# Performance work log

Hardware: AMD Instinct MI355X
Metric: run time of the kernel (lower is better)

## Reference

```python
import jax, jax.numpy as jnp
import numpy as np

NUM_CLASSES = 32
TRI = NUM_CLASSES * (NUM_CLASSES - 1) // 2      # 496 class pairs
HID = 32 * TRI                                  # 15872 total hidden
IN = 512
B = 256
RATIO = 0.0

# pair -> (i, j) class indices, in the same enumeration order as the torch idx formula
_I_IDX, _J_IDX = np.triu_indices(NUM_CLASSES, k=1)
_I_IDX = jnp.asarray(_I_IDX)
_J_IDX = jnp.asarray(_J_IDX)


def setup_inputs() -> dict:
    key = jax.random.key(0)
    ks = jax.random.split(key, 7)
    s = 0.02  # small init so activations stay sane
    return {
        "x": jax.random.normal(ks[0], (B, IN), jnp.float32),
        "W1": jax.random.normal(ks[1], (IN, HID), jnp.float32) * s,
        "b1": jax.random.normal(ks[2], (HID,), jnp.float32) * s,
        "W2": jax.random.normal(ks[3], (HID, HID), jnp.float32) * s,
        "b2": jax.random.normal(ks[4], (HID,), jnp.float32) * s,
        "Wout": jax.random.normal(ks[5], (HID, 2 * TRI), jnp.float32) * s,
        "bout": jax.random.normal(ks[6], (2 * TRI,), jnp.float32) * s,
    }


def reference(x, W1, b1, W2, b2, Wout, bout):
    # MLP stack: fc1 + relu, fc2 + relu (num_layers=2), fc_out
    h = jax.nn.relu(x @ W1 + b1)                 # [B, HID]
    h = jax.nn.relu(h @ W2 + b2)                 # [B, HID]
    out = h @ Wout + bout                        # [B, 2*TRI]

    # vote scatter: out[:, 2p], out[:, 2p+1] are the (i, j) logits of pair p
    pair = out.reshape(B, TRI, 2)                # [B, TRI, 2]
    d = pair[..., 0] - pair[..., 1]              # [B, TRI]
    # original condition: d > ratio  OR  -d >= ratio   (always true at ratio=0)
    mask = (d > RATIO) | (-d >= RATIO)
    vi = jnp.where(mask, pair[..., 0], 0.0)      # contribution to class i
    vj = jnp.where(mask, pair[..., 1], 0.0)      # contribution to class j

    votes = jnp.zeros((B, NUM_CLASSES), jnp.float32)
    votes = votes.at[:, _I_IDX].add(vi)
    votes = votes.at[:, _J_IDX].add(vj)
    return votes
```

## Files before the change

kernel.cpp:

```cpp
#include <hip/hip_runtime.h>
#include <hip/hip_bf16.h>

using short8 = __attribute__((ext_vector_type(8))) short;
using f32x16 = __attribute__((ext_vector_type(16))) float;
using us4    = __attribute__((ext_vector_type(4))) unsigned short;

#define NHID 15872

__device__ __forceinline__ unsigned short f2bf(float f) {
  unsigned u = __builtin_bit_cast(unsigned, f);
  u += 0x7fff + ((u >> 16) & 1);
  return (unsigned short)(u >> 16);
}
__device__ __forceinline__ short f2bf_hw(float f) {
  __hip_bfloat16 h = __float2bfloat16(f);
  return __builtin_bit_cast(short, h);
}
__device__ __forceinline__ float bf2f(unsigned short h) {
  return __builtin_bit_cast(float, ((unsigned)h) << 16);
}

__device__ __forceinline__ void gload16(const void* g, void* l) {
  __builtin_amdgcn_global_load_lds(
      (const __attribute__((address_space(1))) unsigned int*)g,
      (__attribute__((address_space(3))) unsigned int*)l, 16, 0, 0);
}

__device__ __forceinline__ size_t pk_idx(int row, int col) {
  return (size_t)(col >> 4) * 4096 +
         (size_t)(row + 256 * ((col >> 3) & 1)) * 8 + (col & 7);
}

__global__ void cvt_x_pack(const float* __restrict__ x, unsigned short* __restrict__ xpk) {
  int g = blockIdx.x * 256 + threadIdx.x;
  int row = g >> 6, k0 = (g & 63) * 8;
  const float* p = x + (size_t)row * 512 + k0;
  float4 a = *reinterpret_cast<const float4*>(p);
  float4 b = *reinterpret_cast<const float4*>(p + 4);
  us4 o0, o1;
  o0[0] = f2bf(a.x); o0[1] = f2bf(a.y); o0[2] = f2bf(a.z); o0[3] = f2bf(a.w);
  o1[0] = f2bf(b.x); o1[1] = f2bf(b.y); o1[2] = f2bf(b.z); o1[3] = f2bf(b.w);
  unsigned short* d = xpk + pk_idx(row, k0);
  *reinterpret_cast<us4*>(d)     = o0;
  *reinterpret_cast<us4*>(d + 4) = o1;
}


#define WAITV(N) asm volatile("s_waitcnt vmcnt(" #N ")" ::: "memory")

#define STAGEB(BUF, T) do { \
    gload16(bsrc + (size_t)(T) * 32 * NHID,       &Blds[BUF][(w * 4 + 0) * 128]); \
    gload16(bsrc + ((size_t)(T) * 32 + 2) * NHID, &Blds[BUF][(w * 4 + 2) * 128]); \
  } while (0)

#define LOADA(T) do { \
    const unsigned short* ap_ = asrc + (size_t)(T) * 8192; \
    rA[0] = *reinterpret_cast<const short8*>(ap_); \
    rA[1] = *reinterpret_cast<const short8*>(ap_ + 4096); \
    rA[2] = *reinterpret_cast<const short8*>(ap_ + 256); \
    rA[3] = *reinterpret_cast<const short8*>(ap_ + 4096 + 256); \
  } while (0)

#define COMPUTE(BC) do { \
    const float* bb_ = &Blds[BC][0]; \
    _Pragma("unroll") \
    for (int ks_ = 0; ks_ < 2; ++ks_) { \
      short8 bfr_[2]; \
      _Pragma("unroll") \
      for (int nb_ = 0; nb_ < 2; ++nb_) { \
        float tf_[8]; \
        _Pragma("unroll") \
        for (int jj_ = 0; jj_ < 8; ++jj_) \
          tf_[jj_] = bb_[(ks_ * 16 + hi * 8 + jj_) * 128 + wn * 64 + nb_ * 32 + l31]; \
        _Pragma("unroll") \
        for (int jj_ = 0; jj_ < 8; ++jj_) bfr_[nb_][jj_] = f2bf_hw(tf_[jj_]); \
      } \
      acc[0] = __builtin_amdgcn_mfma_f32_32x32x16_bf16(rA[ks_],     bfr_[0], acc[0], 0, 0, 0); \
      acc[1] = __builtin_amdgcn_mfma_f32_32x32x16_bf16(rA[ks_],     bfr_[1], acc[1], 0, 0, 0); \
      acc[2] = __builtin_amdgcn_mfma_f32_32x32x16_bf16(rA[2 + ks_], bfr_[0], acc[2], 0, 0, 0); \
      acc[3] = __builtin_amdgcn_mfma_f32_32x32x16_bf16(rA[2 + ks_], bfr_[1], acc[3], 0, 0, 0); \
    } \
  } while (0)

template<int OUTMODE, bool SWZ>
__global__ __launch_bounds__(512, 4)
void gemm_v12(const unsigned short* __restrict__ Apk, int KC,
              const float* __restrict__ B, const float* __restrict__ bias,
              unsigned short* __restrict__ Cf, float* __restrict__ Cp)
{
  __shared__ float Blds[3][32 * 128];

  int nidx, ks0;
  if (SWZ) {
    int b = blockIdx.x;
    int xcd = b & 7;
    ks0  = xcd >> 1;
    nidx = (b >> 3) * 2 + (xcd & 1);
  } else {
    nidx = blockIdx.x; ks0 = blockIdx.y;
  }
  const int n0   = nidx * 128;
  const int k0   = ks0 * KC;
  const int tid  = threadIdx.x;
  const int w    = tid >> 6;
  const int lane = tid & 63;
  const int l31  = lane & 31;
  const int hi   = lane >> 5;
  const int wm   = w >> 1;
  const int wn   = w & 1;

  f32x16 acc[4] = {};
  short8 rA[4];

  const float* bsrc = B + (size_t)(k0 + w * 4 + hi) * NHID + n0 + l31 * 4;
  const unsigned short* asrc = Apk + (size_t)(k0 >> 4) * 4096 +
                               (size_t)(wm * 64 + l31 + 256 * hi) * 8;

  const int NT = KC >> 5;

  STAGEB(0, 0);
  STAGEB(1, 1);

  int bc = 0;
  for (int t = 0; t < NT; ++t) {
    if (t + 1 < NT) { WAITV(2); } else { WAITV(0); }
    __builtin_amdgcn_sched_barrier(0);
    __builtin_amdgcn_s_barrier();
    LOADA(t);
    if (t + 2 < NT) { int sb_ = bc >= 1 ? bc - 1 : 2; STAGEB(sb_, t + 2); }
    COMPUTE(bc);
    bc = bc == 2 ? 0 : bc + 1;
  }

#pragma unroll
  for (int rb = 0; rb < 2; ++rb) {
#pragma unroll
    for (int nb = 0; nb < 2; ++nb) {
      int col = n0 + wn * 64 + nb * 32 + l31;
      float bv = (OUTMODE != 1) ? bias[col] : 0.f;
#pragma unroll
      for (int reg = 0; reg < 16; ++reg) {
        int row = wm * 64 + rb * 32 + (reg & 3) + 8 * (reg >> 2) + 4 * hi;
        float v = acc[rb * 2 + nb][reg];
        if (OUTMODE == 0) {
          v += bv; v = v > 0.f ? v : 0.f;
          Cf[pk_idx(row, col)] = f2bf(v);
        } else if (OUTMODE == 1) {
          Cp[(size_t)ks0 * 256 * NHID + (size_t)row * NHID + col] = v;
        } else {
          v += bv; v = v > 0.f ? v : 0.f;
          Cf[(size_t)row * NHID + col] = f2bf(v);
        }
      }
    }
  }
}

template<bool PACK>
__global__ void reduce_h(const float* __restrict__ part, const float* __restrict__ bias,
                         unsigned short* __restrict__ out, int S) {
  int g4 = blockIdx.x * 256 + threadIdx.x;
  int row = g4 / 3968;
  int c   = (g4 - row * 3968) * 4;
  size_t off = (size_t)row * NHID + c;
  float4 s = *reinterpret_cast<const float4*>(part + off);
  for (int k = 1; k < S; ++k) {
    float4 p = *reinterpret_cast<const float4*>(part + (size_t)k * 256 * NHID + off);
    s.x += p.x; s.y += p.y; s.z += p.z; s.w += p.w;
  }
  float4 b = *reinterpret_cast<const float4*>(bias + c);
  s.x += b.x; s.y += b.y; s.z += b.z; s.w += b.w;
  us4 o;
  o[0] = f2bf(s.x > 0.f ? s.x : 0.f);
  o[1] = f2bf(s.y > 0.f ? s.y : 0.f);
  o[2] = f2bf(s.z > 0.f ? s.z : 0.f);
  o[3] = f2bf(s.w > 0.f ? s.w : 0.f);
  if (PACK) *reinterpret_cast<us4*>(out + pk_idx(row, c)) = o;
  else      *reinterpret_cast<us4*>(out + off) = o;
}

__global__ void wv_fold(const float* __restrict__ Wout, float* __restrict__ Wv) {
  int g = blockIdx.x * 256 + threadIdx.x;
  int k = g >> 5, c = g & 31;
  const float* row = Wout + (size_t)k * 992;
  float s = 0.f;
#pragma unroll
  for (int o = 0; o < 32; ++o) {
    if (o == c) continue;
    int i = c < o ? c : o;
    int j = c < o ? o : c;
    int p = 31 * i - (i * (i - 1)) / 2 + (j - i - 1);
    s += row[2 * p + (c > o ? 1 : 0)];
  }
  Wv[g] = s;
}

__global__ void votes_partial(const unsigned short* __restrict__ h2,
                              const float* __restrict__ Wv,
                              float* __restrict__ part) {
  int bm = blockIdx.x >> 5;
  int ks = blockIdx.x & 31;
  int r  = bm * 8 + (threadIdx.x >> 5);
  int c  = threadIdx.x & 31;
  const unsigned short* hrow = h2 + (size_t)r * NHID + ks * 496;
  const float* wp = Wv + (size_t)(ks * 496) * 32 + c;
  float s = 0.f;
  for (int k0 = 0; k0 < 496; k0 += 8) {
    short8 hv = *reinterpret_cast<const short8*>(hrow + k0);
#pragma unroll
    for (int j = 0; j < 8; ++j)
      s += bf2f((unsigned short)hv[j]) * wp[(size_t)(k0 + j) * 32];
  }
  part[(size_t)(ks * 256 + r) * 32 + c] = s;
}

__global__ void votes_reduce(const float* __restrict__ part,
                             const float* __restrict__ bout,
                             float* __restrict__ out) {
  int g = blockIdx.x * 256 + threadIdx.x;
  int c = g & 31;
  float s = 0.f;
#pragma unroll
  for (int ks = 0; ks < 32; ++ks) s += part[(size_t)ks * 8192 + g];
  float bv = 0.f;
#pragma unroll
  for (int o = 0; o < 32; ++o) {
    if (o == c) continue;
    int i = c < o ? c : o;
    int j = c < o ? o : c;
    int p = 31 * i - (i * (i - 1)) / 2 + (j - i - 1);
    bv += bout[2 * p + (c > o ? 1 : 0)];
  }
  out[g] = s + bv;
}

extern "C" void kernel_launch(void* const* d_in, const int* in_sizes, int n_in,
                              void* d_out, int out_size, void* d_ws, size_t ws_size,
                              hipStream_t stream) {
  const float* x    = (const float*)d_in[0];
  const float* W1   = (const float*)d_in[1];
  const float* b1   = (const float*)d_in[2];
  const float* W2   = (const float*)d_in[3];
  const float* b2   = (const float*)d_in[4];
  const float* Wout = (const float*)d_in[5];
  const float* bout = (const float*)d_in[6];
  float* out = (float*)d_out;

  char* ws = (char*)d_ws;
  unsigned short* xpk  = (unsigned short*)(ws);
  unsigned short* h1pk = (unsigned short*)(ws + 262144);
  unsigned short* h2   = (unsigned short*)(ws + 8388608);
  float*          Wv   = (float*)(ws + 16515072);
  float*          part = (float*)(ws + 18546688);
  float*         part2 = (float*)(ws + 19595264);

  const size_t PART1 = (size_t)256 * NHID * 4;
  const bool split = ws_size >= 19595264ull + 4 * PART1;

  hipLaunchKernelGGL(cvt_x_pack, dim3(64), dim3(256), 0, stream, x, xpk);
  if (split) {
    hipLaunchKernelGGL((gemm_v12<1, false>), dim3(124, 2), dim3(512), 0, stream,
                       xpk, 256, W1, (const float*)nullptr,
                       (unsigned short*)nullptr, part2);
    hipLaunchKernelGGL((reduce_h<true>), dim3(3968), dim3(256), 0, stream,
                       part2, b1, h1pk, 2);
    hipLaunchKernelGGL((gemm_v12<1, true>), dim3(496), dim3(512), 0, stream,
                       h1pk, 3968, W2, (const float*)nullptr,
                       (unsigned short*)nullptr, part2);
    hipLaunchKernelGGL((reduce_h<false>), dim3(3968), dim3(256), 0, stream,
                       part2, b2, h2, 4);
  } else {
    hipLaunchKernelGGL((gemm_v12<0, false>), dim3(124, 1), dim3(512), 0, stream,
                       xpk, 512, W1, b1, h1pk, (float*)nullptr);
    hipLaunchKernelGGL((gemm_v12<2, false>), dim3(124, 1), dim3(512), 0, stream,
                       h1pk, NHID, W2, b2, h2, (float*)nullptr);
  }
  hipLaunchKernelGGL(wv_fold,       dim3(1984), dim3(256), 0, stream, Wout, Wv);
  hipLaunchKernelGGL(votes_partial, dim3(1024), dim3(256), 0, stream, h2, Wv, part);
  hipLaunchKernelGGL(votes_reduce,  dim3(32),   dim3(256), 0, stream, part, bout, out);
}
```

Measured before the change: 394.0 us.

## Retile GEMM to 128x256 block tiles with K-step 16 and M split

Changes the GEMM block tile from 256 rows x 128 columns to 128 rows x 256 columns, splitting M across a new grid dimension and reducing the K step per stage from 32 to 16. LDS buffers are padded (BSTRIDE) and the B staging pattern now loads two full 256-wide K rows per wave. Each fp32 W row segment is loaded wider and more contiguously, so fewer blocks share a column strip. The trade-off is that each B tile is now read by two M-half blocks, and the pipeline runs more iterations with less MFMA work per barrier.

```diff
diff --git a/kernel.cpp b/kernel.cpp
--- a/kernel.cpp
+++ b/kernel.cpp
@@ -48,75 +48,74 @@
 
 #define WAITV(N) asm volatile("s_waitcnt vmcnt(" #N ")" ::: "memory")
 
+#define BSTRIDE 4736
+
 #define STAGEB(BUF, T) do { \
-    gload16(bsrc + (size_t)(T) * 32 * NHID,       &Blds[BUF][(w * 4 + 0) * 128]); \
-    gload16(bsrc + ((size_t)(T) * 32 + 2) * NHID, &Blds[BUF][(w * 4 + 2) * 128]); \
+    gload16(bsrc + (size_t)(T) * 16 * NHID,       &Blds[(BUF) * BSTRIDE + (2 * w) * 256]); \
+    gload16(bsrc + ((size_t)(T) * 16 + 1) * NHID, &Blds[(BUF) * BSTRIDE + (2 * w + 1) * 256]); \
   } while (0)
 
 #define LOADA(T) do { \
-    const unsigned short* ap_ = asrc + (size_t)(T) * 8192; \
+    const unsigned short* ap_ = asrc + (size_t)(T) * 4096; \
     rA[0] = *reinterpret_cast<const short8*>(ap_); \
-    rA[1] = *reinterpret_cast<const short8*>(ap_ + 4096); \
-    rA[2] = *reinterpret_cast<const short8*>(ap_ + 256); \
-    rA[3] = *reinterpret_cast<const short8*>(ap_ + 4096 + 256); \
+    rA[1] = *reinterpret_cast<const short8*>(ap_ + 256); \
   } while (0)
 
 #define COMPUTE(BC) do { \
-    const float* bb_ = &Blds[BC][0]; \
+    const float* bb_ = &Blds[(BC) * BSTRIDE]; \
+    short8 bfr_[2]; \
     _Pragma("unroll") \
-    for (int ks_ = 0; ks_ < 2; ++ks_) { \
-      short8 bfr_[2]; \
+    for (int nb_ = 0; nb_ < 2; ++nb_) { \
+      float tf_[8]; \
       _Pragma("unroll") \
-      for (int nb_ = 0; nb_ < 2; ++nb_) { \
-        float tf_[8]; \
-        _Pragma("unroll") \
-        for (int jj_ = 0; jj_ < 8; ++jj_) \
-          tf_[jj_] = bb_[(ks_ * 16 + hi * 8 + jj_) * 128 + wn * 64 + nb_ * 32 + l31]; \
-        _Pragma("unroll") \
-        for (int jj_ = 0; jj_ < 8; ++jj_) bfr_[nb_][jj_] = f2bf_hw(tf_[jj_]); \
-      } \
-      acc[0] = __builtin_amdgcn_mfma_f32_32x32x16_bf16(rA[ks_],     bfr_[0], acc[0], 0, 0, 0); \
-      acc[1] = __builtin_amdgcn_mfma_f32_32x32x16_bf16(rA[ks_],     bfr_[1], acc[1], 0, 0, 0); \
-      acc[2] = __builtin_amdgcn_mfma_f32_32x32x16_bf16(rA[2 + ks_], bfr_[0], acc[2], 0, 0, 0); \
-      acc[3] = __builtin_amdgcn_mfma_f32_32x32x16_bf16(rA[2 + ks_], bfr_[1], acc[3], 0, 0, 0); \
+      for (int jj_ = 0; jj_ < 8; ++jj_) \
+        tf_[jj_] = bb_[(hi * 8 + jj_) * 256 + wn * 64 + nb_ * 32 + l31]; \
+      _Pragma("unroll") \
+      for (int jj_ = 0; jj_ < 8; ++jj_) bfr_[nb_][jj_] = f2bf_hw(tf_[jj_]); \
     } \
+    acc[0] = __builtin_amdgcn_mfma_f32_32x32x16_bf16(rA[0], bfr_[0], acc[0], 0, 0, 0); \
+    acc[1] = __builtin_amdgcn_mfma_f32_32x32x16_bf16(rA[0], bfr_[1], acc[1], 0, 0, 0); \
+    acc[2] = __builtin_amdgcn_mfma_f32_32x32x16_bf16(rA[1], bfr_[0], acc[2], 0, 0, 0); \
+    acc[3] = __builtin_amdgcn_mfma_f32_32x32x16_bf16(rA[1], bfr_[1], acc[3], 0, 0, 0); \
   } while (0)
 
 template<int OUTMODE, bool SWZ>
 __global__ __launch_bounds__(512, 4)
-void gemm_v12(const unsigned short* __restrict__ Apk, int KC,
+void gemm_v13(const unsigned short* __restrict__ Apk, int KC,
               const float* __restrict__ B, const float* __restrict__ bias,
               unsigned short* __restrict__ Cf, float* __restrict__ Cp)
 {
-  __shared__ float Blds[3][32 * 128];
-
-  int nidx, ks0;
+  __shared__ float Blds[3 * BSTRIDE];
+
+  int nidx, ks0, mh;
   if (SWZ) {
-    int b = blockIdx.x;
-    int xcd = b & 7;
+    int xs = blockIdx.x;
+    int xcd = xs & 7;
     ks0  = xcd >> 1;
-    nidx = (b >> 3) * 2 + (xcd & 1);
+    nidx = (xs >> 3) * 2 + (xcd & 1);
+    mh   = blockIdx.y;
+    if (nidx >= 62) return;
   } else {
-    nidx = blockIdx.x; ks0 = blockIdx.y;
-  }
-  const int n0   = nidx * 128;
+    nidx = blockIdx.x; mh = blockIdx.y; ks0 = blockIdx.z;
+  }
+  const int n0   = nidx * 256;
   const int k0   = ks0 * KC;
   const int tid  = threadIdx.x;
   const int w    = tid >> 6;
   const int lane = tid & 63;
   const int l31  = lane & 31;
   const int hi   = lane >> 5;
-  const int wm   = w >> 1;
-  const int wn   = w & 1;
+  const int wm   = w >> 2;
+  const int wn   = w & 3;
 
   f32x16 acc[4] = {};
-  short8 rA[4];
-
-  const float* bsrc = B + (size_t)(k0 + w * 4 + hi) * NHID + n0 + l31 * 4;
+  short8 rA[2];
+
+  const float* bsrc = B + (size_t)(k0 + 2 * w) * NHID + n0 + lane * 4;
   const unsigned short* asrc = Apk + (size_t)(k0 >> 4) * 4096 +
-                               (size_t)(wm * 64 + l31 + 256 * hi) * 8;
-
-  const int NT = KC >> 5;
+                               (size_t)(mh * 128 + wm * 64 + l31 + 256 * hi) * 8;
+
+  const int NT = KC >> 4;
 
   STAGEB(0, 0);
   STAGEB(1, 1);
@@ -140,7 +139,7 @@
       float bv = (OUTMODE != 1) ? bias[col] : 0.f;
 #pragma unroll
       for (int reg = 0; reg < 16; ++reg) {
-        int row = wm * 64 + rb * 32 + (reg & 3) + 8 * (reg >> 2) + 4 * hi;
+        int row = mh * 128 + wm * 64 + rb * 32 + (reg & 3) + 8 * (reg >> 2) + 4 * hi;
         float v = acc[rb * 2 + nb][reg];
         if (OUTMODE == 0) {
           v += bv; v = v > 0.f ? v : 0.f;
@@ -259,20 +258,20 @@
 
   hipLaunchKernelGGL(cvt_x_pack, dim3(64), dim3(256), 0, stream, x, xpk);
   if (split) {
-    hipLaunchKernelGGL((gemm_v12<1, false>), dim3(124, 2), dim3(512), 0, stream,
+    hipLaunchKernelGGL((gemm_v13<1, false>), dim3(62, 2, 2), dim3(512), 0, stream,
                        xpk, 256, W1, (const float*)nullptr,
                        (unsigned short*)nullptr, part2);
     hipLaunchKernelGGL((reduce_h<true>), dim3(3968), dim3(256), 0, stream,
                        part2, b1, h1pk, 2);
-    hipLaunchKernelGGL((gemm_v12<1, true>), dim3(496), dim3(512), 0, stream,
+    hipLaunchKernelGGL((gemm_v13<1, true>), dim3(256, 2), dim3(512), 0, stream,
                        h1pk, 3968, W2, (const float*)nullptr,
                        (unsigned short*)nullptr, part2);
     hipLaunchKernelGGL((reduce_h<false>), dim3(3968), dim3(256), 0, stream,
                        part2, b2, h2, 4);
   } else {
-    hipLaunchKernelGGL((gemm_v12<0, false>), dim3(124, 1), dim3(512), 0, stream,
+    hipLaunchKernelGGL((gemm_v13<0, false>), dim3(62, 2, 1), dim3(512), 0, stream,
                        xpk, 512, W1, b1, h1pk, (float*)nullptr);
-    hipLaunchKernelGGL((gemm_v12<2, false>), dim3(124, 1), dim3(512), 0, stream,
+    hipLaunchKernelGGL((gemm_v13<2, false>), dim3(62, 2, 1), dim3(512), 0, stream,
                        h1pk, NHID, W2, b2, h2, (float*)nullptr);
   }
   hipLaunchKernelGGL(wv_fold,       dim3(1984), dim3(256), 0, stream, Wout, Wv);
```

Result: slower. 441.5 us (+12.1%).

## Use 4-wave blocks with 64x128 warp tiles, 16-way split-K, bf16 partials

Applied to the files above, without the earlier changes.

The GEMM moves from 8 waves per block to 4, so each wave computes 64 rows by all 128 columns with 8 accumulators and issues four B staging loads per tile. The W2 GEMM now splits K 16 ways over 1984 blocks instead of 4 ways over 496. Split-K partials are stored as bf16, which halves the partial traffic, and the reduction kernel sums eight elements per thread. The aim is more parallelism in the large GEMM and less partial-sum bandwidth, at the cost of more partial reads in the reduction, extra rounding error from bf16 partials, and higher register pressure. The wait count is now a fixed vmcnt(4) on every iteration, including the last tile.

```diff
diff --git a/kernel.cpp b/kernel.cpp
--- a/kernel.cpp
+++ b/kernel.cpp
@@ -48,10 +48,11 @@
 
 #define WAITV(N) asm volatile("s_waitcnt vmcnt(" #N ")" ::: "memory")
 
-#define STAGEB(BUF, T) do { \
-    gload16(bsrc + (size_t)(T) * 32 * NHID,       &Blds[BUF][(w * 4 + 0) * 128]); \
-    gload16(bsrc + ((size_t)(T) * 32 + 2) * NHID, &Blds[BUF][(w * 4 + 2) * 128]); \
-  } while (0)
+#define STAGEB(BUF, T) do { _Pragma("unroll") \
+  for (int j_ = 0; j_ < 4; ++j_) \
+    gload16(bsrc + ((size_t)(T) * 32 + 2 * j_) * NHID, \
+            &Blds[BUF][(w * 8 + 2 * j_) * 128]); \
+} while (0)
 
 #define LOADA(T) do { \
     const unsigned short* ap_ = asrc + (size_t)(T) * 8192; \
@@ -65,37 +66,34 @@
     const float* bb_ = &Blds[BC][0]; \
     _Pragma("unroll") \
     for (int ks_ = 0; ks_ < 2; ++ks_) { \
-      short8 bfr_[2]; \
       _Pragma("unroll") \
-      for (int nb_ = 0; nb_ < 2; ++nb_) { \
+      for (int nb_ = 0; nb_ < 4; ++nb_) { \
         float tf_[8]; \
         _Pragma("unroll") \
         for (int jj_ = 0; jj_ < 8; ++jj_) \
-          tf_[jj_] = bb_[(ks_ * 16 + hi * 8 + jj_) * 128 + wn * 64 + nb_ * 32 + l31]; \
+          tf_[jj_] = bb_[(ks_ * 16 + hi * 8 + jj_) * 128 + nb_ * 32 + l31]; \
+        short8 bfr_; \
         _Pragma("unroll") \
-        for (int jj_ = 0; jj_ < 8; ++jj_) bfr_[nb_][jj_] = f2bf_hw(tf_[jj_]); \
+        for (int jj_ = 0; jj_ < 8; ++jj_) bfr_[jj_] = f2bf_hw(tf_[jj_]); \
+        acc[nb_]     = __builtin_amdgcn_mfma_f32_32x32x16_bf16(rA[ks_],     bfr_, acc[nb_],     0, 0, 0); \
+        acc[4 + nb_] = __builtin_amdgcn_mfma_f32_32x32x16_bf16(rA[2 + ks_], bfr_, acc[4 + nb_], 0, 0, 0); \
       } \
-      acc[0] = __builtin_amdgcn_mfma_f32_32x32x16_bf16(rA[ks_],     bfr_[0], acc[0], 0, 0, 0); \
-      acc[1] = __builtin_amdgcn_mfma_f32_32x32x16_bf16(rA[ks_],     bfr_[1], acc[1], 0, 0, 0); \
-      acc[2] = __builtin_amdgcn_mfma_f32_32x32x16_bf16(rA[2 + ks_], bfr_[0], acc[2], 0, 0, 0); \
-      acc[3] = __builtin_amdgcn_mfma_f32_32x32x16_bf16(rA[2 + ks_], bfr_[1], acc[3], 0, 0, 0); \
     } \
   } while (0)
 
 template<int OUTMODE, bool SWZ>
-__global__ __launch_bounds__(512, 4)
-void gemm_v12(const unsigned short* __restrict__ Apk, int KC,
+__global__ __launch_bounds__(256, 3)
+void gemm_v14(const unsigned short* __restrict__ Apk, int KC,
               const float* __restrict__ B, const float* __restrict__ bias,
-              unsigned short* __restrict__ Cf, float* __restrict__ Cp)
+              unsigned short* __restrict__ Cf, unsigned short* __restrict__ Cpb)
 {
   __shared__ float Blds[3][32 * 128];
 
   int nidx, ks0;
   if (SWZ) {
     int b = blockIdx.x;
-    int xcd = b & 7;
-    ks0  = xcd >> 1;
-    nidx = (b >> 3) * 2 + (xcd & 1);
+    ks0  = b & 15;
+    nidx = b >> 4;
   } else {
     nidx = blockIdx.x; ks0 = blockIdx.y;
   }
@@ -106,15 +104,13 @@
   const int lane = tid & 63;
   const int l31  = lane & 31;
   const int hi   = lane >> 5;
-  const int wm   = w >> 1;
-  const int wn   = w & 1;
-
-  f32x16 acc[4] = {};
+
+  f32x16 acc[8] = {};
   short8 rA[4];
 
-  const float* bsrc = B + (size_t)(k0 + w * 4 + hi) * NHID + n0 + l31 * 4;
+  const float* bsrc = B + (size_t)(k0 + w * 8 + hi) * NHID + n0 + l31 * 4;
   const unsigned short* asrc = Apk + (size_t)(k0 >> 4) * 4096 +
-                               (size_t)(wm * 64 + l31 + 256 * hi) * 8;
+                               (size_t)(w * 64 + l31 + 256 * hi) * 8;
 
   const int NT = KC >> 5;
 
@@ -123,7 +119,7 @@
 
   int bc = 0;
   for (int t = 0; t < NT; ++t) {
-    if (t + 1 < NT) { WAITV(2); } else { WAITV(0); }
+    WAITV(4);
     __builtin_amdgcn_sched_barrier(0);
     __builtin_amdgcn_s_barrier();
     LOADA(t);
@@ -135,18 +131,18 @@
 #pragma unroll
   for (int rb = 0; rb < 2; ++rb) {
 #pragma unroll
-    for (int nb = 0; nb < 2; ++nb) {
-      int col = n0 + wn * 64 + nb * 32 + l31;
+    for (int nb = 0; nb < 4; ++nb) {
+      int col = n0 + nb * 32 + l31;
       float bv = (OUTMODE != 1) ? bias[col] : 0.f;
 #pragma unroll
       for (int reg = 0; reg < 16; ++reg) {
-        int row = wm * 64 + rb * 32 + (reg & 3) + 8 * (reg >> 2) + 4 * hi;
-        float v = acc[rb * 2 + nb][reg];
+        int row = w * 64 + rb * 32 + (reg & 3) + 8 * (reg >> 2) + 4 * hi;
+        float v = acc[rb * 4 + nb][reg];
         if (OUTMODE == 0) {
           v += bv; v = v > 0.f ? v : 0.f;
           Cf[pk_idx(row, col)] = f2bf(v);
         } else if (OUTMODE == 1) {
-          Cp[(size_t)ks0 * 256 * NHID + (size_t)row * NHID + col] = v;
+          Cpb[(size_t)ks0 * 256 * NHID + (size_t)row * NHID + col] = f2bf(v);
         } else {
           v += bv; v = v > 0.f ? v : 0.f;
           Cf[(size_t)row * NHID + col] = f2bf(v);
@@ -157,26 +153,28 @@
 }
 
 template<bool PACK>
-__global__ void reduce_h(const float* __restrict__ part, const float* __restrict__ bias,
-                         unsigned short* __restrict__ out, int S) {
-  int g4 = blockIdx.x * 256 + threadIdx.x;
-  int row = g4 / 3968;
-  int c   = (g4 - row * 3968) * 4;
+__global__ void reduce_hb(const unsigned short* __restrict__ part,
+                          const float* __restrict__ bias,
+                          unsigned short* __restrict__ out, int S) {
+  int g8 = blockIdx.x * 256 + threadIdx.x;
+  int row = g8 / 1984;
+  int c   = (g8 - row * 1984) * 8;
   size_t off = (size_t)row * NHID + c;
-  float4 s = *reinterpret_cast<const float4*>(part + off);
-  for (int k = 1; k < S; ++k) {
-    float4 p = *reinterpret_cast<const float4*>(part + (size_t)k * 256 * NHID + off);
-    s.x += p.x; s.y += p.y; s.z += p.z; s.w += p.w;
-  }
-  float4 b = *reinterpret_cast<const float4*>(bias + c);
-  s.x += b.x; s.y += b.y; s.z += b.z; s.w += b.w;
-  us4 o;
-  o[0] = f2bf(s.x > 0.f ? s.x : 0.f);
-  o[1] = f2bf(s.y > 0.f ? s.y : 0.f);
-  o[2] = f2bf(s.z > 0.f ? s.z : 0.f);
-  o[3] = f2bf(s.w > 0.f ? s.w : 0.f);
-  if (PACK) *reinterpret_cast<us4*>(out + pk_idx(row, c)) = o;
-  else      *reinterpret_cast<us4*>(out + off) = o;
+  float s[8] = {0.f, 0.f, 0.f, 0.f, 0.f, 0.f, 0.f, 0.f};
+  for (int k = 0; k < S; ++k) {
+    short8 p = *reinterpret_cast<const short8*>(part + (size_t)k * 256 * NHID + off);
+#pragma unroll
+    for (int j = 0; j < 8; ++j) s[j] += bf2f((unsigned short)p[j]);
+  }
+  short8 o;
+#pragma unroll
+  for (int j = 0; j < 8; ++j) {
+    float v = s[j] + bias[c + j];
+    v = v > 0.f ? v : 0.f;
+    o[j] = (short)f2bf(v);
+  }
+  if (PACK) *reinterpret_cast<short8*>(out + pk_idx(row, c)) = o;
+  else      *reinterpret_cast<short8*>(out + off) = o;
 }
 
 __global__ void wv_fold(const float* __restrict__ Wout, float* __restrict__ Wv) {
@@ -252,28 +250,28 @@
   unsigned short* h2   = (unsigned short*)(ws + 8388608);
   float*          Wv   = (float*)(ws + 16515072);
   float*          part = (float*)(ws + 18546688);
-  float*         part2 = (float*)(ws + 19595264);
-
-  const size_t PART1 = (size_t)256 * NHID * 4;
-  const bool split = ws_size >= 19595264ull + 4 * PART1;
+  unsigned short* pb   = (unsigned short*)(ws + 19595264);
+
+  const size_t PARTB = (size_t)256 * NHID * 2;
+  const bool split = ws_size >= 19595264ull + 16 * PARTB;
 
   hipLaunchKernelGGL(cvt_x_pack, dim3(64), dim3(256), 0, stream, x, xpk);
   if (split) {
-    hipLaunchKernelGGL((gemm_v12<1, false>), dim3(124, 2), dim3(512), 0, stream,
+    hipLaunchKernelGGL((gemm_v14<1, false>), dim3(124, 2), dim3(256), 0, stream,
                        xpk, 256, W1, (const float*)nullptr,
-                       (unsigned short*)nullptr, part2);
-    hipLaunchKernelGGL((reduce_h<true>), dim3(3968), dim3(256), 0, stream,
-                       part2, b1, h1pk, 2);
-    hipLaunchKernelGGL((gemm_v12<1, true>), dim3(496), dim3(512), 0, stream,
-                       h1pk, 3968, W2, (const float*)nullptr,
-                       (unsigned short*)nullptr, part2);
-    hipLaunchKernelGGL((reduce_h<false>), dim3(3968), dim3(256), 0, stream,
-                       part2, b2, h2, 4);
+                       (unsigned short*)nullptr, pb);
+    hipLaunchKernelGGL((reduce_hb<true>), dim3(1984), dim3(256), 0, stream,
+                       pb, b1, h1pk, 2);
+    hipLaunchKernelGGL((gemm_v14<1, true>), dim3(1984), dim3(256), 0, stream,
+                       h1pk, 992, W2, (const float*)nullptr,
+                       (unsigned short*)nullptr, pb);
+    hipLaunchKernelGGL((reduce_hb<false>), dim3(1984), dim3(256), 0, stream,
+                       pb, b2, h2, 16);
   } else {
-    hipLaunchKernelGGL((gemm_v12<0, false>), dim3(124, 1), dim3(512), 0, stream,
-                       xpk, 512, W1, b1, h1pk, (float*)nullptr);
-    hipLaunchKernelGGL((gemm_v12<2, false>), dim3(124, 1), dim3(512), 0, stream,
-                       h1pk, NHID, W2, b2, h2, (float*)nullptr);
+    hipLaunchKernelGGL((gemm_v14<0, false>), dim3(124, 1), dim3(256), 0, stream,
+                       xpk, 512, W1, b1, h1pk, (unsigned short*)nullptr);
+    hipLaunchKernelGGL((gemm_v14<2, false>), dim3(124, 1), dim3(256), 0, stream,
+                       h1pk, NHID, W2, b2, h2, (unsigned short*)nullptr);
   }
   hipLaunchKernelGGL(wv_fold,       dim3(1984), dim3(256), 0, stream, Wout, Wv);
   hipLaunchKernelGGL(votes_partial, dim3(1024), dim3(256), 0, stream, h2, Wv, part);
```

After: 449.8 us. 14.2% more time.
